# Performance work log

Hardware: AMD Instinct MI355X
Metric: run time of the kernel (lower is better)

Reference implementation:

```python
import jax, jax.numpy as jnp
import numpy as np
from jax import lax

B, T, D, H, V, L = 32, 64, 512, 512, 32000, 2
EOS, PAD = 3, 0
SAMPLE_SEED = 42


def setup_inputs() -> dict:
    key = jax.random.key(0)
    ks = jax.random.split(key, 10)
    s = 0.05
    return {
        "input_seq": jax.random.normal(ks[0], (B, T, D), dtype=jnp.float32),
        "h_encode": jax.random.normal(ks[1], (L, B, H), dtype=jnp.float32),
        "c_encode": jax.random.normal(ks[2], (L, B, H), dtype=jnp.float32),
        # stacked per-layer LSTM cell params (layer0 in=D, layer>=1 in=H; D==H so stackable)
        "W_ih": jax.random.normal(ks[3], (L, 4 * H, D), dtype=jnp.float32) * s,
        "W_hh": jax.random.normal(ks[4], (L, 4 * H, H), dtype=jnp.float32) * s,
        "b_ih": jnp.zeros((L, 4 * H), dtype=jnp.float32),
        "b_hh": jnp.zeros((L, 4 * H), dtype=jnp.float32),
        "fc_w": jax.random.normal(ks[5], (V, H), dtype=jnp.float32) * s,
        "fc_b": jnp.zeros((V,), dtype=jnp.float32),
        "embed": jax.random.normal(ks[6], (V, D), dtype=jnp.float32) * s,
    }


def _lstm_cell(x, h, c, wi, wh, bi, bh):
    # gates in torch LSTMCell order: i, f, g, o
    g = x @ wi.T + bi + h @ wh.T + bh  # [B, 4H]
    i, f, gg, o = jnp.split(g, 4, axis=-1)
    i, f, o = jax.nn.sigmoid(i), jax.nn.sigmoid(f), jax.nn.sigmoid(o)
    c2 = f * c + i * jnp.tanh(gg)
    h2 = o * jnp.tanh(c2)
    return h2, c2


def reference(input_seq, h_encode, c_encode, W_ih, W_hh, b_ih, b_hh, fc_w, fc_b, embed):
    n_layers = h_encode.shape[0]
    seq = jnp.swapaxes(input_seq, 0, 1)  # [T, B, D]
    batch = input_seq.shape[0]

    def step(carry, t):
        h, c, finished, x = carry
        inp = x
        hs, cs = [], []
        for l in range(n_layers):  # fixed small layer loop
            hl, cl = _lstm_cell(inp, h[l], c[l], W_ih[l], W_hh[l], b_ih[l], b_hh[l])
            hs.append(hl)
            cs.append(cl)
            inp = hl
        h2 = jnp.stack(hs)
        c2 = jnp.stack(cs)
        logits = inp @ fc_w.T + fc_b  # [B, V]; temperature=1.0 is identity
        key = jax.random.fold_in(jax.random.key(SAMPLE_SEED), t)
        sampled = jax.random.categorical(key, logits, axis=-1)  # multinomial(softmax(logits))
        token = jnp.where(finished, PAD, sampled)
        finished2 = finished | (sampled == EOS)
        next_x = embed[token]  # [B, D] feedback embedding (no teacher forcing)
        return (h2, c2, finished2, next_x), (logits, token)

    carry0 = (h_encode, c_encode, jnp.zeros((batch,), dtype=bool), seq[0])
    _, (logits_t, tokens_t) = lax.scan(step, carry0, jnp.arange(seq.shape[0]))
    outputs = jnp.swapaxes(logits_t, 0, 1)  # [B, T, V]
    tokens = jnp.swapaxes(tokens_t, 0, 1)  # [B, T]
    return outputs, tokens
```

## Files before the change

kernel.cpp:

```cpp
#include <hip/hip_runtime.h>
#include <cstdint>
#include <cstddef>

#define B_  32
#define T_  64
#define D_  512
#define H_  512
#define V_  32000
#define GATES 2048

__device__ float g_h[2][2 * B_ * H_];
__device__ float g_c[2][2 * B_ * H_];
__device__ int   g_fin[2][B_];
__device__ unsigned long long g_best[B_];
__device__ float g_wT[125 * 512 * 256];
__device__ float g_wLT[2][1024 * 2048];
__device__ float g_part0[16][B_][GATES];
__device__ float g_part1[24][B_][GATES];
__device__ float g_lpart[8][B_][V_];

__host__ __device__ __forceinline__ void threefry2x32(uint32_t k0, uint32_t k1,
                                                      uint32_t x0, uint32_t x1,
                                                      uint32_t& o0, uint32_t& o1) {
  uint32_t kx = k0 ^ k1 ^ 0x1BD11BDAu;
  x0 += k0; x1 += k1;
#define RND(r) { x0 += x1; x1 = (x1 << (r)) | (x1 >> (32 - (r))); x1 ^= x0; }
  RND(13) RND(15) RND(26) RND(6)  x0 += k1; x1 += kx + 1u;
  RND(17) RND(29) RND(16) RND(24) x0 += kx; x1 += k0 + 2u;
  RND(13) RND(15) RND(26) RND(6)  x0 += k0; x1 += k1 + 3u;
  RND(17) RND(29) RND(16) RND(24) x0 += k1; x1 += kx + 4u;
  RND(13) RND(15) RND(26) RND(6)  x0 += kx; x1 += k0 + 5u;
#undef RND
  o0 = x0; o1 = x1;
}

__device__ __forceinline__ float gumbel_from_u32(uint32_t bits) {
  float f = __uint_as_float((bits >> 9) | 0x3f800000u) - 1.0f;
  const float TINY = 1.1754943508222875e-38f;
  float u = f * (1.0f - TINY) + TINY;
  u = fmaxf(u, TINY);
  return -logf(-logf(u));
}

__device__ __forceinline__ int unpack_v(unsigned long long bb) {
  int v = (int)(0xFFFFFFFFu - (uint32_t)(bb & 0xFFFFFFFFu));
  if (v < 0) v = 0;
  if (v >= V_) v = V_ - 1;
  return v;
}

__global__ void init_kernel(const float* __restrict__ h_enc,
                            const float* __restrict__ c_enc) {
  int i = blockIdx.x * 256 + threadIdx.x;
  if (i < 2 * B_ * H_) { g_h[0][i] = h_enc[i]; g_c[0][i] = c_enc[i]; }
  if (i < B_) { g_fin[0][i] = 0; g_fin[1][i] = 0; g_best[i] = 0ull; }
}

__global__ void transpose_kernel(const float* __restrict__ src, int R, int which) {
  float* dst;
  switch (which) {
    case 0:  dst = g_wT; break;
    case 1:  dst = g_wLT[0]; break;
    case 2:  dst = g_wLT[0] + 512 * 2048; break;
    case 3:  dst = g_wLT[1]; break;
    default: dst = g_wLT[1] + 512 * 2048; break;
  }
  __shared__ float tile[64][65];
  const int r0 = blockIdx.x * 64;
  const int c0 = blockIdx.y * 64;
  const int tx = threadIdx.x & 63;
  const int ty = threadIdx.x >> 6;
#pragma unroll
  for (int i = 0; i < 16; ++i) {
    const int row = ty + 4 * i;
    tile[row][tx] = src[(size_t)(r0 + row) * 512 + c0 + tx];
  }
  __syncthreads();
#pragma unroll
  for (int i = 0; i < 16; ++i) {
    const int row = ty + 4 * i;
    const int k = c0 + row, v = r0 + tx;
    if (which == 0) {
      dst[(size_t)(v >> 8) * (512 * 256) + (size_t)k * 256 + (v & 255)] =
          tile[tx][row];
    } else {
      dst[(size_t)k * R + v] = tile[tx][row];
    }
  }
}

template<int PER>
__device__ __forceinline__ void stage_t(float* __restrict__ zs,
                                        const float* __restrict__ row,
                                        int kq, int b) {
#pragma unroll
  for (int i = 0; i < PER; i += 4) {
    const float4 v = *(const float4*)&row[kq * PER + i];
    const int kk = kq * PER + i;
    zs[(kk + 0) * 32 + b] = v.x;
    zs[(kk + 1) * 32 + b] = v.y;
    zs[(kk + 2) * 32 + b] = v.z;
    zs[(kk + 3) * 32 + b] = v.w;
  }
}

template<int KS>
__device__ __forceinline__ void mm_part(const float* __restrict__ wrow,
                                        float* __restrict__ pout,
                                        const float* __restrict__ zs,
                                        int j0, int tid) {
  float2 acc[32];
#pragma unroll
  for (int b = 0; b < 32; ++b) acc[b] = make_float2(0.f, 0.f);
#pragma unroll 4
  for (int k = 0; k < KS; ++k) {
    const float2 w = *(const float2*)&wrow[(size_t)k * GATES + j0 + 2 * tid];
    const float4* z4 = (const float4*)&zs[k * 32];
#pragma unroll
    for (int bq = 0; bq < 8; ++bq) {
      const float4 z = z4[bq];
      acc[bq * 4 + 0].x += w.x * z.x; acc[bq * 4 + 0].y += w.y * z.x;
      acc[bq * 4 + 1].x += w.x * z.y; acc[bq * 4 + 1].y += w.y * z.y;
      acc[bq * 4 + 2].x += w.x * z.z; acc[bq * 4 + 2].y += w.y * z.z;
      acc[bq * 4 + 3].x += w.x * z.w; acc[bq * 4 + 3].y += w.y * z.w;
    }
  }
#pragma unroll
  for (int b = 0; b < 32; ++b)
    *(float2*)&pout[(size_t)b * GATES + j0 + 2 * tid] = acc[b];
}

__global__ void parts_a_kernel(int cur, int t,
                               const float* __restrict__ input_seq,
                               const float* __restrict__ embed,
                               float* __restrict__ out_tokens) {
  __shared__ __align__(16) float zs[64 * 32];
  __shared__ int stok[B_];
  const int tid = threadIdx.x;
  const int blk = blockIdx.x;
  const int b = tid >> 3, kq = tid & 7;

  if (blk < 64) {
    const int ks = blk >> 2, jt = blk & 3;
    const int k0 = ks * 64, j0 = jt * 512;
    if (k0 < 512) {
      if (t == 0) {
        const float* row = &input_seq[(size_t)b * (T_ * D_)];
        stage_t<8>(zs, row + k0, kq, b);
      } else {
        if (tid < B_) {
          unsigned long long bb = g_best[tid];
          int v = unpack_v(bb);
          int fin = g_fin[(t + 1) & 1][tid];
          int tok = fin ? 0 : v;
          stok[tid] = tok;
          if (blk == 0) {
            out_tokens[(size_t)tid * T_ + (t - 1)] = (float)tok;
            g_fin[t & 1][tid] = fin | (v == 3 ? 1 : 0);
          }
        }
        __syncthreads();
        const float* row = &embed[(size_t)stok[b] * D_];
        stage_t<8>(zs, row + k0, kq, b);
      }
    } else {
      const float* row = &g_h[cur][0 * B_ * H_ + b * H_];
      stage_t<8>(zs, row + (k0 - 512), kq, b);
    }
    __syncthreads();
    mm_part<64>(&g_wLT[0][(size_t)k0 * GATES], &g_part0[ks][0][0], zs, j0, tid);
  } else {
    const int bb2 = blk - 64;
    const int ks = bb2 >> 2, jt = bb2 & 3;
    const int k0 = ks * 64, j0 = jt * 512;
    const float* row = &g_h[cur][1 * B_ * H_ + b * H_];
    stage_t<8>(zs, row + k0, kq, b);
    __syncthreads();
    mm_part<64>(&g_wLT[1][(size_t)(512 + k0) * GATES], &g_part1[16 + ks][0][0],
                zs, j0, tid);
  }
}

__global__ void parts_l1x_kernel(int cur) {
  __shared__ __align__(16) float zs[32 * 32];
  const int tid = threadIdx.x;
  const int ks = blockIdx.x >> 2, jt = blockIdx.x & 3;
  const int k0 = ks * 32, j0 = jt * 512;
  const int b = tid >> 3, kq = tid & 7;
  const float* row = &g_h[cur ^ 1][0 * B_ * H_ + b * H_];
  stage_t<4>(zs, row + k0, kq, b);
  __syncthreads();
  mm_part<32>(&g_wLT[1][(size_t)k0 * GATES], &g_part1[ks][0][0], zs, j0, tid);
}

__global__ void lstm_finish_kernel(int cur, int layer, int nslots,
                                   const float* __restrict__ bih,
                                   const float* __restrict__ bhh) {
  const int gid = blockIdx.x * 256 + threadIdx.x;
  const int b = gid >> 9, j = gid & 511;
  const float* P = (layer == 0) ? &g_part0[0][0][0] : &g_part1[0][0][0];
  float gi = 0.f, gf = 0.f, gg = 0.f, go = 0.f;
  for (int s = 0; s < nslots; ++s) {
    const float* p = P + (size_t)s * B_ * GATES + (size_t)b * GATES;
    gi += p[j];
    gf += p[512 + j];
    gg += p[1024 + j];
    go += p[1536 + j];
  }
  gi += bih[j]        + bhh[j];
  gf += bih[512 + j]  + bhh[512 + j];
  gg += bih[1024 + j] + bhh[1024 + j];
  go += bih[1536 + j] + bhh[1536 + j];

  const float* c_in = &g_c[cur][layer * B_ * H_];
  float* h_out = &g_h[cur ^ 1][layer * B_ * H_];
  float* c_out = &g_c[cur ^ 1][layer * B_ * H_];
  float c0 = c_in[b * H_ + j];
  float si = 1.f / (1.f + expf(-gi));
  float sf = 1.f / (1.f + expf(-gf));
  float so = 1.f / (1.f + expf(-go));
  float cn = sf * c0 + si * tanhf(gg);
  float hn = so * tanhf(cn);
  c_out[b * H_ + j] = cn;
  h_out[b * H_ + j] = hn;
}

__global__ __launch_bounds__(256) void logits_part_kernel(int cur) {
  __shared__ __align__(16) float hs[64 * 32];
  const int blk = blockIdx.x;
  const int vt = blk % 125, ks = blk / 125;
  const int tid = threadIdx.x;
  const int k0 = ks * 64;

  if (blk == 0 && tid < B_) g_best[tid] = 0ull;

  {
    const int b = tid >> 3, kq = tid & 7;
    const float* row = &g_h[cur ^ 1][B_ * H_ + b * H_];
    stage_t<8>(hs, row + k0, kq, b);
  }
  __syncthreads();

  const int vp = tid & 63, bg = tid >> 6;
  const int vl = vp * 4;
  const float* wbase = &g_wT[(size_t)vt * (512 * 256) + (size_t)k0 * 256 + vl];

  float4 acc[8];
#pragma unroll
  for (int i = 0; i < 8; ++i) acc[i] = make_float4(0.f, 0.f, 0.f, 0.f);

#define FMA4(A, S) { A.x += w.x*(S); A.y += w.y*(S); A.z += w.z*(S); A.w += w.w*(S); }
#pragma unroll 8
  for (int k = 0; k < 64; ++k) {
    const float4 w   = *(const float4*)&wbase[(size_t)k * 256];
    const float4 zlo = *(const float4*)&hs[k * 32 + bg * 8];
    const float4 zhi = *(const float4*)&hs[k * 32 + bg * 8 + 4];
    FMA4(acc[0], zlo.x) FMA4(acc[1], zlo.y) FMA4(acc[2], zlo.z) FMA4(acc[3], zlo.w)
    FMA4(acc[4], zhi.x) FMA4(acc[5], zhi.y) FMA4(acc[6], zhi.z) FMA4(acc[7], zhi.w)
  }
#undef FMA4

  const int v = vt * 256 + vl;
#pragma unroll
  for (int i = 0; i < 8; ++i)
    *(float4*)&g_lpart[ks][bg * 8 + i][v] = acc[i];
}

__global__ __launch_bounds__(256) void logits_combine_kernel(
    const float* __restrict__ fc_b, float* __restrict__ out_logits,
    int t, uint32_t key0, uint32_t key1) {
  __shared__ unsigned long long sv[256];
  const int b  = blockIdx.x >> 4;
  const int vr = blockIdx.x & 15;
  const int tid = threadIdx.x;
  const int vbase = vr * 2000, vend = vbase + 2000;

  unsigned long long best = 0ull;
  for (int it = 0; it < 4; ++it) {
    const int v = vbase + (it * 256 + tid) * 2;
    if (v < vend) {
      float sx = 0.f, sy = 0.f;
#pragma unroll
      for (int ks = 0; ks < 8; ++ks) {
        const float2 p = *(const float2*)&g_lpart[ks][b][v];
        sx += p.x; sy += p.y;
      }
      const float l0 = sx + fc_b[v];
      const float l1 = sy + fc_b[v + 1];
      *(float2*)&out_logits[(size_t)(b * T_ + t) * V_ + v] = make_float2(l0, l1);
      uint32_t y0, y1;
      threefry2x32(key0, key1, 0u, (uint32_t)(b * V_ + v), y0, y1);
      const float val0 = l0 + gumbel_from_u32(y0 ^ y1);
      threefry2x32(key0, key1, 0u, (uint32_t)(b * V_ + v + 1), y0, y1);
      const float val1 = l1 + gumbel_from_u32(y0 ^ y1);
      uint32_t u0 = __float_as_uint(val0);
      u0 ^= (u0 >> 31) ? 0xFFFFFFFFu : 0x80000000u;
      uint32_t u1 = __float_as_uint(val1);
      u1 ^= (u1 >> 31) ? 0xFFFFFFFFu : 0x80000000u;
      const unsigned long long p0 =
          ((unsigned long long)u0 << 32) | (unsigned long long)(0xFFFFFFFFu - (uint32_t)v);
      const unsigned long long p1 =
          ((unsigned long long)u1 << 32) | (unsigned long long)(0xFFFFFFFFu - (uint32_t)(v + 1));
      unsigned long long pk = p0 > p1 ? p0 : p1;
      if (pk > best) best = pk;
    }
  }
  sv[tid] = best;
  __syncthreads();
  for (int s = 128; s > 0; s >>= 1) {
    if (tid < s) { if (sv[tid + s] > sv[tid]) sv[tid] = sv[tid + s]; }
    __syncthreads();
  }
  if (tid == 0) atomicMax(&g_best[b], sv[0]);
}

__global__ void finalize_kernel(float* __restrict__ out_tokens) {
  const int tid = threadIdx.x;
  if (tid < B_) {
    int v = unpack_v(g_best[tid]);
    int fin = g_fin[(T_ + 1) & 1][tid];
    int tok = fin ? 0 : v;
    out_tokens[(size_t)tid * T_ + (T_ - 1)] = (float)tok;
  }
}

extern "C" void kernel_launch(void* const* d_in, const int* in_sizes, int n_in,
                              void* d_out, int out_size, void* d_ws, size_t ws_size,
                              hipStream_t stream) {
  const float* input_seq = (const float*)d_in[0];
  const float* h_enc = (const float*)d_in[1];
  const float* c_enc = (const float*)d_in[2];
  const float* Wih   = (const float*)d_in[3];
  const float* Whh   = (const float*)d_in[4];
  const float* bih   = (const float*)d_in[5];
  const float* bhh   = (const float*)d_in[6];
  const float* fc_w  = (const float*)d_in[7];
  const float* fc_b  = (const float*)d_in[8];
  const float* embed = (const float*)d_in[9];
  float* out = (float*)d_out;
  float* tok_out = out + (size_t)B_ * T_ * V_;
  (void)d_ws; (void)ws_size; (void)in_sizes; (void)n_in; (void)out_size;

  init_kernel<<<128, 256, 0, stream>>>(h_enc, c_enc);

  transpose_kernel<<<dim3(500, 8), 256, 0, stream>>>(fc_w, 32000, 0);
  transpose_kernel<<<dim3(32, 8),  256, 0, stream>>>(Wih,                      2048, 1);
  transpose_kernel<<<dim3(32, 8),  256, 0, stream>>>(Whh,                      2048, 2);
  transpose_kernel<<<dim3(32, 8),  256, 0, stream>>>(Wih + (size_t)2048 * 512, 2048, 3);
  transpose_kernel<<<dim3(32, 8),  256, 0, stream>>>(Whh + (size_t)2048 * 512, 2048, 4);

  uint32_t keys[T_][2];
  for (int t = 0; t < T_; ++t)
    threefry2x32(0u, 42u, 0u, (uint32_t)t, keys[t][0], keys[t][1]);

  int cur = 0;
  for (int t = 0; t < T_; ++t) {
    parts_a_kernel<<<96, 256, 0, stream>>>(cur, t, input_seq, embed, tok_out);
    lstm_finish_kernel<<<64, 256, 0, stream>>>(cur, 0, 16, bih, bhh);
    parts_l1x_kernel<<<64, 256, 0, stream>>>(cur);
    lstm_finish_kernel<<<64, 256, 0, stream>>>(cur, 1, 24, bih + 2048, bhh + 2048);
    logits_part_kernel<<<1000, 256, 0, stream>>>(cur);
    logits_combine_kernel<<<512, 256, 0, stream>>>(fc_b, out, t, keys[t][0], keys[t][1]);
    cur ^= 1;
  }
  finalize_kernel<<<1, 64, 0, stream>>>(tok_out);
}
```

Baseline: 5.247 ms.

## Fuse layer-0 LSTM finish into layer-1 input GEMM and shard argmax slots

The layer-0 gate reduction and nonlinearity are folded into the kernel that computes the layer-1 input projection. Each block recomputes the h values it needs for its k-slice directly into shared memory, which removes one kernel launch per timestep at the cost of redundant gate math across the four j-tiles. The per-batch argmax atomic target is also split into 8 double-buffered slots that are reduced by the consumer. This lowers atomic contention and removes the reset from the logits kernel.

Result: no change. 5.156 ms (median of 2 runs) (-1.7%).

```diff
diff --git a/kernel.cpp b/kernel.cpp
--- a/kernel.cpp
+++ b/kernel.cpp
@@ -12,7 +12,7 @@
 __device__ float g_h[2][2 * B_ * H_];
 __device__ float g_c[2][2 * B_ * H_];
 __device__ int   g_fin[2][B_];
-__device__ unsigned long long g_best[B_];
+__device__ unsigned long long g_best2[2][B_][8];
 __device__ float g_wT[125 * 512 * 256];
 __device__ float g_wLT[2][1024 * 2048];
 __device__ float g_part0[16][B_][GATES];
@@ -49,11 +49,17 @@
   return v;
 }
 
+__device__ __forceinline__ unsigned long long ullmax(unsigned long long a,
+                                                     unsigned long long b) {
+  return a > b ? a : b;
+}
+
 __global__ void init_kernel(const float* __restrict__ h_enc,
                             const float* __restrict__ c_enc) {
   int i = blockIdx.x * 256 + threadIdx.x;
   if (i < 2 * B_ * H_) { g_h[0][i] = h_enc[i]; g_c[0][i] = c_enc[i]; }
-  if (i < B_) { g_fin[0][i] = 0; g_fin[1][i] = 0; g_best[i] = 0ull; }
+  if (i < B_) { g_fin[0][i] = 0; g_fin[1][i] = 0; }
+  if (i < 2 * B_ * 8) ((unsigned long long*)g_best2)[i] = 0ull;
 }
 
 __global__ void transpose_kernel(const float* __restrict__ src, int R, int which) {
@@ -149,8 +155,11 @@
         stage_t<8>(zs, row + k0, kq, b);
       } else {
         if (tid < B_) {
-          unsigned long long bb = g_best[tid];
-          int v = unpack_v(bb);
+          const int ps = (t - 1) & 1;
+          unsigned long long m = 0ull;
+#pragma unroll
+          for (int s = 0; s < 8; ++s) m = ullmax(m, g_best2[ps][tid][s]);
+          int v = unpack_v(m);
           int fin = g_fin[(t + 1) & 1][tid];
           int tok = fin ? 0 : v;
           stok[tid] = tok;
@@ -159,6 +168,8 @@
             g_fin[t & 1][tid] = fin | (v == 3 ? 1 : 0);
           }
         }
+        if (blk == 0)
+          g_best2[t & 1][tid >> 3][tid & 7] = 0ull;
         __syncthreads();
         const float* row = &embed[(size_t)stok[b] * D_];
         stage_t<8>(zs, row + k0, kq, b);
@@ -181,14 +192,43 @@
   }
 }
 
-__global__ void parts_l1x_kernel(int cur) {
+__global__ __launch_bounds__(256) void finish0_l1x_kernel(
+    int cur, const float* __restrict__ bih, const float* __restrict__ bhh) {
   __shared__ __align__(16) float zs[32 * 32];
   const int tid = threadIdx.x;
   const int ks = blockIdx.x >> 2, jt = blockIdx.x & 3;
   const int k0 = ks * 32, j0 = jt * 512;
-  const int b = tid >> 3, kq = tid & 7;
-  const float* row = &g_h[cur ^ 1][0 * B_ * H_ + b * H_];
-  stage_t<4>(zs, row + k0, kq, b);
+
+#pragma unroll
+  for (int i = 0; i < 4; ++i) {
+    const int idx = tid + i * 256;
+    const int b = idx >> 5, jl = idx & 31;
+    const int j = k0 + jl;
+    float gi = 0.f, gf = 0.f, gg = 0.f, go = 0.f;
+    for (int s = 0; s < 16; ++s) {
+      const float* p = &g_part0[s][b][0];
+      gi += p[j];
+      gf += p[512 + j];
+      gg += p[1024 + j];
+      go += p[1536 + j];
+    }
+    gi += bih[j]        + bhh[j];
+    gf += bih[512 + j]  + bhh[512 + j];
+    gg += bih[1024 + j] + bhh[1024 + j];
+    go += bih[1536 + j] + bhh[1536 + j];
+
+    const float c0v = g_c[cur][0 * B_ * H_ + b * H_ + j];
+    const float si = 1.f / (1.f + expf(-gi));
+    const float sf = 1.f / (1.f + expf(-gf));
+    const float so = 1.f / (1.f + expf(-go));
+    const float cn = sf * c0v + si * tanhf(gg);
+    const float hn = so * tanhf(cn);
+    zs[jl * 32 + b] = hn;
+    if (jt == 0) {
+      g_c[cur ^ 1][0 * B_ * H_ + b * H_ + j] = cn;
+      g_h[cur ^ 1][0 * B_ * H_ + b * H_ + j] = hn;
+    }
+  }
   __syncthreads();
   mm_part<32>(&g_wLT[1][(size_t)k0 * GATES], &g_part1[ks][0][0], zs, j0, tid);
 }
@@ -212,17 +252,14 @@
   gg += bih[1024 + j] + bhh[1024 + j];
   go += bih[1536 + j] + bhh[1536 + j];
 
-  const float* c_in = &g_c[cur][layer * B_ * H_];
-  float* h_out = &g_h[cur ^ 1][layer * B_ * H_];
-  float* c_out = &g_c[cur ^ 1][layer * B_ * H_];
-  float c0 = c_in[b * H_ + j];
-  float si = 1.f / (1.f + expf(-gi));
-  float sf = 1.f / (1.f + expf(-gf));
-  float so = 1.f / (1.f + expf(-go));
-  float cn = sf * c0 + si * tanhf(gg);
-  float hn = so * tanhf(cn);
-  c_out[b * H_ + j] = cn;
-  h_out[b * H_ + j] = hn;
+  const float c0 = g_c[cur][layer * B_ * H_ + b * H_ + j];
+  const float si = 1.f / (1.f + expf(-gi));
+  const float sf = 1.f / (1.f + expf(-gf));
+  const float so = 1.f / (1.f + expf(-go));
+  const float cn = sf * c0 + si * tanhf(gg);
+  const float hn = so * tanhf(cn);
+  g_c[cur ^ 1][layer * B_ * H_ + b * H_ + j] = cn;
+  g_h[cur ^ 1][layer * B_ * H_ + b * H_ + j] = hn;
 }
 
 __global__ __launch_bounds__(256) void logits_part_kernel(int cur) {
@@ -231,8 +268,6 @@
   const int vt = blk % 125, ks = blk / 125;
   const int tid = threadIdx.x;
   const int k0 = ks * 64;
-
-  if (blk == 0 && tid < B_) g_best[tid] = 0ull;
 
   {
     const int b = tid >> 3, kq = tid & 7;
@@ -311,16 +346,19 @@
     if (tid < s) { if (sv[tid + s] > sv[tid]) sv[tid] = sv[tid + s]; }
     __syncthreads();
   }
-  if (tid == 0) atomicMax(&g_best[b], sv[0]);
+  if (tid == 0) atomicMax(&g_best2[t & 1][b][vr & 7], sv[0]);
 }
 
 __global__ void finalize_kernel(float* __restrict__ out_tokens) {
   const int tid = threadIdx.x;
   if (tid < B_) {
-    int v = unpack_v(g_best[tid]);
-    int fin = g_fin[(T_ + 1) & 1][tid];
-    int tok = fin ? 0 : v;
-    out_tokens[(size_t)tid * T_ + (T_ - 1)] = (float)tok;
+    const int ps = (T_ - 1) & 1;
+    unsigned long long m = 0ull;
+#pragma unroll
+    for (int s = 0; s < 8; ++s) m = ullmax(m, g_best2[ps][tid][s]);
+    const int v = unpack_v(m);
+    const int fin = g_fin[(T_ + 1) & 1][tid];
+    out_tokens[(size_t)tid * T_ + (T_ - 1)] = (float)(fin ? 0 : v);
   }
 }
 
@@ -356,11 +394,11 @@
   int cur = 0;
   for (int t = 0; t < T_; ++t) {
     parts_a_kernel<<<96, 256, 0, stream>>>(cur, t, input_seq, embed, tok_out);
-    lstm_finish_kernel<<<64, 256, 0, stream>>>(cur, 0, 16, bih, bhh);
-    parts_l1x_kernel<<<64, 256, 0, stream>>>(cur);
+    finish0_l1x_kernel<<<64, 256, 0, stream>>>(cur, bih, bhh);
     lstm_finish_kernel<<<64, 256, 0, stream>>>(cur, 1, 24, bih + 2048, bhh + 2048);
     logits_part_kernel<<<1000, 256, 0, stream>>>(cur);
-    logits_combine_kernel<<<512, 256, 0, stream>>>(fc_b, out, t, keys[t][0], keys[t][1]);
+    logits_combine_kernel<<<512, 256, 0, stream>>>(fc_b, out, t,
+                                                   keys[t][0], keys[t][1]);
     cur ^= 1;
   }
   finalize_kernel<<<1, 64, 0, stream>>>(tok_out);
```
